# Kernel optimization log

Hardware: AMD Instinct MI355X
Metric: run time of the kernel (lower is better)

## Reference

```python
import jax, jax.numpy as jnp
import numpy as np

B, S, DM = 8, 1024, 512   # batch, seq_len, model dim
H, D = 8, 64              # n_heads, per-head dim


def setup_inputs() -> dict:
    key = jax.random.key(0)
    k1, k2, k3, k4, k5 = jax.random.split(key, 5)
    sc = 1.0 / np.sqrt(DM)
    return {
        "x": jax.random.normal(k1, (B, S, DM), dtype=jnp.float32),
        "Wq": jax.random.normal(k2, (H, DM, D), dtype=jnp.float32) * sc,
        "Wk": jax.random.normal(k3, (H, DM, D), dtype=jnp.float32) * sc,
        "Wv": jax.random.normal(k4, (H, DM, D), dtype=jnp.float32) * sc,
        "Wo": jax.random.normal(k5, (H * D, DM), dtype=jnp.float32) * (1.0 / np.sqrt(H * D)),
    }


def reference(x, Wq, Wk, Wv, Wo):
    # Batched multi-head attention equivalent to the per-head Python loop.
    q = jnp.einsum("bsm,hmd->bhsd", x, Wq)
    k = jnp.einsum("bsm,hmd->bhsd", x, Wk)
    v = jnp.einsum("bsm,hmd->bhsd", x, Wv)
    scores = jnp.einsum("bhsd,bhtd->bhst", q, k) / jnp.sqrt(jnp.float32(D))
    attn = jax.nn.softmax(scores, axis=-1)          # [B,H,S,S]
    heads = jnp.einsum("bhst,bhtd->bhsd", attn, v)  # [B,H,S,D]
    # concat heads along feature dim (head order matches loop order)
    concat = heads.transpose(0, 2, 1, 3).reshape(B, S, H * D)
    z = jnp.einsum("bsf,fm->bsm", concat, Wo)       # output projection
    return z, attn
```

## Files before the change

kernel.cpp:

```cpp
#include <hip/hip_runtime.h>

#define B 8
#define S 1024
#define DM 512
#define H 8
#define D 64

typedef __attribute__((ext_vector_type(8))) short bf16x8;
typedef __attribute__((ext_vector_type(4))) float f32x4;

__device__ inline f32x4 mfma16(bf16x8 a, bf16x8 b, f32x4 c) {
  return __builtin_amdgcn_mfma_f32_16x16x32_bf16(a, b, c, 0, 0, 0);
}

__device__ inline ushort f2bf(float f) {
  uint u = __float_as_uint(f);
  u += 0x7fff + ((u >> 16) & 1);
  return (ushort)(u >> 16);
}

#define GLOAD16(gp, lp)                                                  \
  __builtin_amdgcn_global_load_lds(                                      \
      (const __attribute__((address_space(1))) void*)(gp),               \
      (__attribute__((address_space(3))) void*)(lp), 16, 0, 0)

__global__ __launch_bounds__(256) void prep_kernel(
    const float* __restrict__ x, const float* __restrict__ Wq,
    const float* __restrict__ Wk, const float* __restrict__ Wv,
    const float* __restrict__ Wo, ushort* __restrict__ xbf,
    ushort* __restrict__ WT, ushort* __restrict__ WoT) {
  const int bid = blockIdx.x;
  if (bid < 4096) {
    int idx = bid * 256 + threadIdx.x;
    float4 v = *(const float4*)(x + (size_t)idx * 4);
    ushort4 o;
    o.x = f2bf(v.x); o.y = f2bf(v.y); o.z = f2bf(v.z); o.w = f2bf(v.w);
    *(ushort4*)(xbf + (size_t)idx * 4) = o;
  } else if (bid < 7168) {
    int idx = (bid - 4096) * 256 + threadIdx.x;
    int g = idx >> 18;
    int rem = idx & 262143;
    const float* W = (g == 0) ? Wq : (g == 1) ? Wk : Wv;
    float val = W[rem];
    int d = rem & 63, m = (rem >> 6) & 511, h = rem >> 15;
    WT[((size_t)(g << 9) + (h << 6) + d) * 512 + m] = f2bf(val);
  } else {
    int idx = (bid - 7168) * 256 + threadIdx.x;
    int m = idx & 511, f = idx >> 9;
    WoT[(size_t)m * 512 + f] = f2bf(Wo[(size_t)f * DM + m]);
  }
}

__global__ __launch_bounds__(256) void qkv_gemm_kernel(
    const ushort* __restrict__ A, const ushort* __restrict__ Bm,
    ushort* __restrict__ qb, ushort* __restrict__ kb, ushort* __restrict__ vt) {
  __shared__ ushort As[128 * 64], Bs[128 * 64];
  const int tid = threadIdx.x;
  const int m0 = blockIdx.x * 128, n0 = blockIdx.y * 128;
  const int w = tid >> 6, l = tid & 63;
  const int r = l & 15, q = l >> 4;
  const int wr = (w >> 1) * 64, wc = (w & 1) * 64;

  f32x4 acc[4][4] = {};
  const int o0 = tid * 16;

  for (int k0 = 0; k0 < 512; k0 += 64) {
    __syncthreads();
    #pragma unroll
    for (int j = 0; j < 4; ++j) {
      int o = j * 4096 + o0;
      int row = o >> 7, cb = o & 127;
      GLOAD16(A + (size_t)(m0 + row) * 512 + k0 + (cb >> 1), &As[o >> 1]);
      GLOAD16(Bm + (size_t)(n0 + row) * 512 + k0 + (cb >> 1), &Bs[o >> 1]);
    }
    __syncthreads();
    #pragma unroll
    for (int kk = 0; kk < 64; kk += 32) {
      bf16x8 fa[4], fb[4];
      #pragma unroll
      for (int mi = 0; mi < 4; ++mi)
        fa[mi] = *(const bf16x8*)&As[(wr + mi * 16 + r) * 64 + kk + q * 8];
      #pragma unroll
      for (int nj = 0; nj < 4; ++nj)
        fb[nj] = *(const bf16x8*)&Bs[(wc + nj * 16 + r) * 64 + kk + q * 8];
      #pragma unroll
      for (int mi = 0; mi < 4; ++mi)
        #pragma unroll
        for (int nj = 0; nj < 4; ++nj)
          acc[mi][nj] = mfma16(fa[mi], fb[nj], acc[mi][nj]);
    }
  }

  const int g = n0 >> 9;
  #pragma unroll
  for (int mi = 0; mi < 4; ++mi)
    #pragma unroll
    for (int nj = 0; nj < 4; ++nj)
      #pragma unroll
      for (int i = 0; i < 4; ++i) {
        int row = m0 + wr + mi * 16 + q * 4 + i;
        int col = n0 + wc + nj * 16 + r;
        int bb = row >> 10, s = row & 1023;
        int fl = col & 511, h = fl >> 6, d = fl & 63;
        ushort val = f2bf(acc[mi][nj][i]);
        if (g == 0)
          qb[(((size_t)bb * H + h) * S + s) * D + d] = val;
        else if (g == 1)
          kb[(((size_t)bb * H + h) * S + s) * D + d] = val;
        else
          vt[(((size_t)bb * H + h) * D + d) * S + s] = val;
      }
}

__global__ __launch_bounds__(256, 4) void attn_kernel(
    const ushort* __restrict__ qb, const ushort* __restrict__ kb,
    const ushort* __restrict__ vt, float* __restrict__ attn,
    ushort* __restrict__ concat) {
  __shared__ ushort Pl[16 * 1024];
  __shared__ float redm[4][16], redsum[4][16];
  const int tid = threadIdx.x;
  const int w = tid >> 6, l = tid & 63;
  const int r = l & 15, q = l >> 4;
  const int s0 = blockIdx.x * 16, bh = blockIdx.y;

  const ushort* qp = qb + ((size_t)bh * S + s0) * D;
  bf16x8 qa0 = *(const bf16x8*)(qp + r * 64 + q * 8);
  bf16x8 qa1 = *(const bf16x8*)(qp + r * 64 + 32 + q * 8);

  const ushort* kp = kb + (size_t)bh * S * D;
  f32x4 sc[16];
  #pragma unroll
  for (int kt = 0; kt < 16; ++kt) {
    const ushort* kr = kp + (size_t)(w * 256 + kt * 16 + r) * 64 + q * 8;
    bf16x8 kf0 = *(const bf16x8*)kr;
    bf16x8 kf1 = *(const bf16x8*)(kr + 32);
    f32x4 a = {};
    a = mfma16(qa0, kf0, a);
    a = mfma16(qa1, kf1, a);
    sc[kt] = a * 0.125f;
  }

  float mx[4];
  #pragma unroll
  for (int i = 0; i < 4; ++i) {
    float m = sc[0][i];
    #pragma unroll
    for (int kt = 1; kt < 16; ++kt) m = fmaxf(m, sc[kt][i]);
    #pragma unroll
    for (int msk = 1; msk < 16; msk <<= 1) m = fmaxf(m, __shfl_xor(m, msk));
    mx[i] = m;
  }
  if (r == 0) {
    #pragma unroll
    for (int i = 0; i < 4; ++i) redm[w][q * 4 + i] = mx[i];
  }
  __syncthreads();
  #pragma unroll
  for (int i = 0; i < 4; ++i)
    mx[i] = fmaxf(fmaxf(redm[0][q * 4 + i], redm[1][q * 4 + i]),
                  fmaxf(redm[2][q * 4 + i], redm[3][q * 4 + i]));

  float sm[4] = {0.f, 0.f, 0.f, 0.f};
  #pragma unroll
  for (int kt = 0; kt < 16; ++kt)
    #pragma unroll
    for (int i = 0; i < 4; ++i) {
      float e = __expf(sc[kt][i] - mx[i]);
      sc[kt][i] = e;
      sm[i] += e;
    }
  #pragma unroll
  for (int i = 0; i < 4; ++i) {
    float s = sm[i];
    #pragma unroll
    for (int msk = 1; msk < 16; msk <<= 1) s += __shfl_xor(s, msk);
    sm[i] = s;
  }
  if (r == 0) {
    #pragma unroll
    for (int i = 0; i < 4; ++i) redsum[w][q * 4 + i] = sm[i];
  }
  __syncthreads();
  float rinv[4];
  #pragma unroll
  for (int i = 0; i < 4; ++i)
    rinv[i] = 1.0f / (redsum[0][q * 4 + i] + redsum[1][q * 4 + i] +
                      redsum[2][q * 4 + i] + redsum[3][q * 4 + i]);

  float* ap = attn + ((size_t)bh * S + s0) * S;
  #pragma unroll
  for (int kt = 0; kt < 16; ++kt) {
    int col = w * 256 + kt * 16 + r;
    #pragma unroll
    for (int i = 0; i < 4; ++i) {
      int row = q * 4 + i;
      ap[(size_t)row * S + col] = sc[kt][i] * rinv[i];
      Pl[row * 1024 + (col ^ ((row & 7) << 3))] = f2bf(sc[kt][i]);
    }
  }
  __syncthreads();

  {
    const int d0 = w * 16;
    const ushort* vp = vt + ((size_t)bh * D + d0 + r) * S;
    f32x4 acc[4] = {};
    #pragma unroll
    for (int stp = 0; stp < 32; ++stp) {
      int t0 = stp * 32 + q * 8;
      bf16x8 pa = *(const bf16x8*)&Pl[r * 1024 + (t0 ^ ((r & 7) << 3))];
      bf16x8 vb = *(const bf16x8*)(vp + t0);
      acc[stp & 3] = mfma16(pa, vb, acc[stp & 3]);
    }
    f32x4 tot = acc[0] + acc[1] + acc[2] + acc[3];
    const int b = bh >> 3, h = bh & 7;
    #pragma unroll
    for (int i = 0; i < 4; ++i)
      concat[((size_t)b * S + s0 + q * 4 + i) * DM + h * D + d0 + r] =
          f2bf(tot[i] * rinv[i]);
  }
}

__global__ __launch_bounds__(256) void outproj_gemm_kernel(
    const ushort* __restrict__ A, const ushort* __restrict__ Bm,
    float* __restrict__ z) {
  __shared__ ushort As[128 * 64], Bs[128 * 64];
  const int tid = threadIdx.x;
  const int m0 = blockIdx.x * 128, n0 = blockIdx.y * 128;
  const int w = tid >> 6, l = tid & 63;
  const int r = l & 15, q = l >> 4;
  const int wr = (w >> 1) * 64, wc = (w & 1) * 64;

  f32x4 acc[4][4] = {};
  const int o0 = tid * 16;

  for (int k0 = 0; k0 < 512; k0 += 64) {
    __syncthreads();
    #pragma unroll
    for (int j = 0; j < 4; ++j) {
      int o = j * 4096 + o0;
      int row = o >> 7, cb = o & 127;
      GLOAD16(A + (size_t)(m0 + row) * 512 + k0 + (cb >> 1), &As[o >> 1]);
      GLOAD16(Bm + (size_t)(n0 + row) * 512 + k0 + (cb >> 1), &Bs[o >> 1]);
    }
    __syncthreads();
    #pragma unroll
    for (int kk = 0; kk < 64; kk += 32) {
      bf16x8 fa[4], fb[4];
      #pragma unroll
      for (int mi = 0; mi < 4; ++mi)
        fa[mi] = *(const bf16x8*)&As[(wr + mi * 16 + r) * 64 + kk + q * 8];
      #pragma unroll
      for (int nj = 0; nj < 4; ++nj)
        fb[nj] = *(const bf16x8*)&Bs[(wc + nj * 16 + r) * 64 + kk + q * 8];
      #pragma unroll
      for (int mi = 0; mi < 4; ++mi)
        #pragma unroll
        for (int nj = 0; nj < 4; ++nj)
          acc[mi][nj] = mfma16(fa[mi], fb[nj], acc[mi][nj]);
    }
  }

  #pragma unroll
  for (int mi = 0; mi < 4; ++mi)
    #pragma unroll
    for (int nj = 0; nj < 4; ++nj)
      #pragma unroll
      for (int i = 0; i < 4; ++i) {
        int row = m0 + wr + mi * 16 + q * 4 + i;
        int col = n0 + wc + nj * 16 + r;
        z[(size_t)row * DM + col] = acc[mi][nj][i];
      }
}

extern "C" void kernel_launch(void* const* d_in, const int* in_sizes, int n_in,
                              void* d_out, int out_size, void* d_ws, size_t ws_size,
                              hipStream_t stream) {
  const float* x  = (const float*)d_in[0];
  const float* Wq = (const float*)d_in[1];
  const float* Wk = (const float*)d_in[2];
  const float* Wv = (const float*)d_in[3];
  const float* Wo = (const float*)d_in[4];

  float* z    = (float*)d_out;
  float* attn = z + (size_t)B * S * DM;

  ushort* xbf    = (ushort*)d_ws;
  ushort* WT     = xbf + (size_t)8192 * 512;
  ushort* WoT    = WT + (size_t)1536 * 512;
  ushort* qb     = WoT + (size_t)512 * 512;
  ushort* kb     = qb + (size_t)B * H * S * D;
  ushort* vt     = kb + (size_t)B * H * S * D;
  ushort* concat = vt + (size_t)B * H * S * D;

  prep_kernel<<<8192, 256, 0, stream>>>(x, Wq, Wk, Wv, Wo, xbf, WT, WoT);
  qkv_gemm_kernel<<<dim3(8192 / 128, 1536 / 128), 256, 0, stream>>>(
      xbf, WT, qb, kb, vt);
  attn_kernel<<<dim3(S / 16, B * H), 256, 0, stream>>>(
      qb, kb, vt, attn, concat);
  outproj_gemm_kernel<<<dim3(8192 / 128, 512 / 128), 256, 0, stream>>>(
      concat, WoT, z);
}
```

Baseline: 199.8 us.

## Shrink output-projection GEMM tiles to 64x64 with padded LDS and register staging

Measured after the change: 195.4 us. -2.2%, faster.

```diff
diff --git a/kernel.cpp b/kernel.cpp
--- a/kernel.cpp
+++ b/kernel.cpp
@@ -223,51 +223,50 @@
 __global__ __launch_bounds__(256) void outproj_gemm_kernel(
     const ushort* __restrict__ A, const ushort* __restrict__ Bm,
     float* __restrict__ z) {
-  __shared__ ushort As[128 * 64], Bs[128 * 64];
+  __shared__ ushort As[64][72], Bs[64][72];
   const int tid = threadIdx.x;
-  const int m0 = blockIdx.x * 128, n0 = blockIdx.y * 128;
+  const int m0 = blockIdx.x * 64, n0 = blockIdx.y * 64;
   const int w = tid >> 6, l = tid & 63;
   const int r = l & 15, q = l >> 4;
-  const int wr = (w >> 1) * 64, wc = (w & 1) * 64;
-
-  f32x4 acc[4][4] = {};
-  const int o0 = tid * 16;
+  const int mh = (w >> 1) * 32, nh = (w & 1) * 32;
+
+  f32x4 acc[2][2] = {};
+  const int srow = tid >> 2, sco = (tid & 3) * 16;
 
   for (int k0 = 0; k0 < 512; k0 += 64) {
+    const ushort* ap = A + (size_t)(m0 + srow) * 512 + k0 + sco;
+    const ushort* bp = Bm + (size_t)(n0 + srow) * 512 + k0 + sco;
+    uint4 a0 = *(const uint4*)ap;
+    uint4 a1 = *(const uint4*)(ap + 8);
+    uint4 b0 = *(const uint4*)bp;
+    uint4 b1 = *(const uint4*)(bp + 8);
     __syncthreads();
-    #pragma unroll
-    for (int j = 0; j < 4; ++j) {
-      int o = j * 4096 + o0;
-      int row = o >> 7, cb = o & 127;
-      GLOAD16(A + (size_t)(m0 + row) * 512 + k0 + (cb >> 1), &As[o >> 1]);
-      GLOAD16(Bm + (size_t)(n0 + row) * 512 + k0 + (cb >> 1), &Bs[o >> 1]);
-    }
+    *(uint4*)&As[srow][sco] = a0;
+    *(uint4*)&As[srow][sco + 8] = a1;
+    *(uint4*)&Bs[srow][sco] = b0;
+    *(uint4*)&Bs[srow][sco + 8] = b1;
     __syncthreads();
     #pragma unroll
     for (int kk = 0; kk < 64; kk += 32) {
-      bf16x8 fa[4], fb[4];
-      #pragma unroll
-      for (int mi = 0; mi < 4; ++mi)
-        fa[mi] = *(const bf16x8*)&As[(wr + mi * 16 + r) * 64 + kk + q * 8];
-      #pragma unroll
-      for (int nj = 0; nj < 4; ++nj)
-        fb[nj] = *(const bf16x8*)&Bs[(wc + nj * 16 + r) * 64 + kk + q * 8];
-      #pragma unroll
-      for (int mi = 0; mi < 4; ++mi)
-        #pragma unroll
-        for (int nj = 0; nj < 4; ++nj)
-          acc[mi][nj] = mfma16(fa[mi], fb[nj], acc[mi][nj]);
-    }
-  }
-
-  #pragma unroll
-  for (int mi = 0; mi < 4; ++mi)
-    #pragma unroll
-    for (int nj = 0; nj < 4; ++nj)
+      bf16x8 fa0 = *(const bf16x8*)&As[mh + r][kk + q * 8];
+      bf16x8 fa1 = *(const bf16x8*)&As[mh + 16 + r][kk + q * 8];
+      bf16x8 fb0 = *(const bf16x8*)&Bs[nh + r][kk + q * 8];
+      bf16x8 fb1 = *(const bf16x8*)&Bs[nh + 16 + r][kk + q * 8];
+      acc[0][0] = mfma16(fa0, fb0, acc[0][0]);
+      acc[0][1] = mfma16(fa0, fb1, acc[0][1]);
+      acc[1][0] = mfma16(fa1, fb0, acc[1][0]);
+      acc[1][1] = mfma16(fa1, fb1, acc[1][1]);
+    }
+  }
+
+  #pragma unroll
+  for (int mi = 0; mi < 2; ++mi)
+    #pragma unroll
+    for (int nj = 0; nj < 2; ++nj)
       #pragma unroll
       for (int i = 0; i < 4; ++i) {
-        int row = m0 + wr + mi * 16 + q * 4 + i;
-        int col = n0 + wc + nj * 16 + r;
+        int row = m0 + mh + mi * 16 + q * 4 + i;
+        int col = n0 + nh + nj * 16 + r;
         z[(size_t)row * DM + col] = acc[mi][nj][i];
       }
 }
@@ -297,6 +296,6 @@
       xbf, WT, qb, kb, vt);
   attn_kernel<<<dim3(S / 16, B * H), 256, 0, stream>>>(
       qb, kb, vt, attn, concat);
-  outproj_gemm_kernel<<<dim3(8192 / 128, 512 / 128), 256, 0, stream>>>(
+  outproj_gemm_kernel<<<dim3(8192 / 64, 512 / 64), 256, 0, stream>>>(
       concat, WoT, z);
 }
```
